# Kernel optimization log

Measured on AMD Instinct MI355X. Metric: run time of the kernel, lower is better.

## Reference

```python
import jax, jax.numpy as jnp
import numpy as np


def _segment_sum(x):
    # x: (..., T). Returns (..., T, T) with [i, j] = sum_{j < k <= i} x[k] for i >= j, else -inf.
    T = x.shape[-1]
    lower = jnp.tril(jnp.ones((T, T), dtype=bool), -1)
    xx = jnp.where(lower, x[..., :, None], 0.0)  # [..., i, j] = x[..., i] for i > j
    seg = jnp.cumsum(xx, axis=-2)
    keep = jnp.tril(jnp.ones((T, T), dtype=bool), 0)
    return jnp.where(keep, seg, -jnp.inf)


def _ssd(x, dt, A, B, C, chunk_len, D):
    # x: (b,s,H,dh)  dt: (b,s,H)  A: (H,)  B,C: (b,s,H,N)
    b, s, H, dh = x.shape
    N = B.shape[-1]
    c = s // chunk_len  # seq_len multiple of chunk_len -> pad_size == 0
    D_res = D[..., None] * x
    x = x * dt[..., None]
    Adt = A.astype(x.dtype) * dt  # (b,s,H)
    xc = x.reshape(b, c, chunk_len, H, dh)
    Ac = Adt.reshape(b, c, chunk_len, H).transpose(0, 3, 1, 2)  # (b,H,c,L)
    Bc = B.reshape(b, c, chunk_len, H, N)
    Cc = C.reshape(b, c, chunk_len, H, N)
    A_cumsum = jnp.cumsum(Ac, axis=-1)  # (b,H,c,L)
    Lmat = jnp.exp(_segment_sum(Ac))  # (b,H,c,L,L)
    # intra-chunk (diagonal) term
    Gm = jnp.einsum('bclhn,bcshn->bclsh', Cc, Bc)
    M = Gm * Lmat.transpose(0, 2, 3, 4, 1)  # (b,c,L,L,H)
    Y_diag = jnp.einsum('bclsh,bcshd->bclhd', M, xc)
    # chunk states
    decay_states = jnp.exp(A_cumsum[..., -1:] - A_cumsum)  # (b,H,c,L)
    B_decay = Bc * decay_states.transpose(0, 2, 3, 1)[..., None]
    states = jnp.einsum('bclhn,bclhd->bchdn', B_decay, xc)  # (b,c,H,dh,N)
    states = jnp.concatenate([jnp.zeros_like(states[:, :1]), states], axis=1)  # (b,c+1,H,dh,N)
    decay_chunk = jnp.exp(_segment_sum(jnp.pad(A_cumsum[..., -1], ((0, 0), (0, 0), (1, 0)))))  # (b,H,c+1,c+1)
    # Faithful to the source module: (decay[...,None,None] * states[:, :, None]).sum(dim=2)
    # sums over the z (row) axis -> equivalent to scaling states by the column sums of decay_chunk.
    col_sum = decay_chunk.sum(axis=2)  # (b,H,c+1)
    new_states = states * col_sum.transpose(0, 2, 1)[..., None, None]  # (b,c+1,H,dh,N)
    states = new_states[:, :-1]  # (b,c,H,dh,N)
    # inter-chunk (off-diagonal) term
    Y_off = jnp.einsum('bclhn,bchdn->bclhd', Cc, states) * jnp.exp(A_cumsum).transpose(0, 2, 3, 1)[..., None]
    return (Y_diag + Y_off).reshape(b, s, H, dh) + D_res


def setup_inputs() -> dict:
    key = jax.random.key(0)
    ks = jax.random.split(key, 6)
    b, s, dm, H, N, G = 2, 2048, 2048, 32, 128, 8
    sc = 0.02
    return {
        'hidden_states': jax.random.normal(ks[0], (b, s, dm), jnp.float32),
        'A_log': jnp.log(jnp.arange(1, H + 1, dtype=jnp.float32)),
        'D': jnp.ones((H,), jnp.float32),
        'W_B': jax.random.normal(ks[1], (dm, G * N), jnp.float32) * sc,
        'b_B': jnp.zeros((G * N,), jnp.float32),
        'W_C': jax.random.normal(ks[2], (dm, G * N), jnp.float32) * sc,
        'b_C': jnp.zeros((G * N,), jnp.float32),
        'W_x': jax.random.normal(ks[3], (dm, dm), jnp.float32) * sc,
        'b_x': jnp.zeros((dm,), jnp.float32),
        'W_dt': jax.random.normal(ks[4], (dm, H), jnp.float32) * sc,
        'b_dt': jnp.zeros((H,), jnp.float32),
        'W_out': jax.random.normal(ks[5], (dm, dm), jnp.float32) * sc,
        'b_out': jnp.zeros((dm,), jnp.float32),
        'chunk_len': 256,
        'd_state': 128,
    }


def reference(hidden_states, A_log, D, W_B, b_B, W_C, b_C, W_x, b_x, W_dt, b_dt, W_out, b_out, chunk_len, d_state):
    b, s, dm = hidden_states.shape
    H = A_log.shape[0]
    G = W_B.shape[1] // d_state
    A = -jnp.exp(A_log)
    Bm = (hidden_states @ W_B + b_B).reshape(b, s, G, d_state)
    Bm = jnp.tile(Bm, (1, 1, H // G, 1))  # torch .repeat tiles groups over heads
    Cm = (hidden_states @ W_C + b_C).reshape(b, s, G, d_state)
    Cm = jnp.tile(Cm, (1, 1, H // G, 1))
    dt = jax.nn.softplus(hidden_states @ W_dt + b_dt)  # (b,s,H)
    x = (hidden_states @ W_x + b_x).reshape(b, s, H, dm // H)
    y = _ssd(x, dt, A, Bm, Cm, chunk_len, D)
    return y.reshape(b, s, dm) @ W_out + b_out
```

## Files before the change

### kernel.cpp

```cpp
#include <hip/hip_runtime.h>

#define S_   2048
#define BB   2
#define MR   4096
#define DM   2048
#define HH   32
#define DH   64
#define GG   8
#define NST  128
#define NC   8
#define LCH  256
#define KD   2048

typedef __attribute__((ext_vector_type(4))) float f32x4;
typedef __attribute__((ext_vector_type(8))) short bf16x8;

typedef __attribute__((address_space(1))) const void gvoid;
typedef __attribute__((address_space(3))) void lvoid;

__device__ __forceinline__ short f2bf(float f) {
  unsigned u = __builtin_bit_cast(unsigned, f);
  u += 0x7FFFu + ((u >> 16) & 1u);
  return (short)(u >> 16);
}
__device__ __forceinline__ float bf2f(short s) {
  unsigned u = ((unsigned)(unsigned short)s) << 16;
  return __builtin_bit_cast(float, u);
}
__device__ __forceinline__ unsigned pack2(short lo, short hi) {
  return (unsigned)(unsigned short)lo | ((unsigned)(unsigned short)hi << 16);
}

__global__ void k_cast(const float* __restrict__ src, short* __restrict__ dst, int n8) {
  int i = blockIdx.x * 256 + threadIdx.x;
  if (i >= n8) return;
  const float4 a = *(const float4*)(src + (size_t)i * 8);
  const float4 b = *(const float4*)(src + (size_t)i * 8 + 4);
  uint4 o;
  o.x = pack2(f2bf(a.x), f2bf(a.y));
  o.y = pack2(f2bf(a.z), f2bf(a.w));
  o.z = pack2(f2bf(b.x), f2bf(b.y));
  o.w = pack2(f2bf(b.z), f2bf(b.w));
  *(uint4*)(dst + (size_t)i * 8) = o;
}

__global__ __launch_bounds__(256) void k_cast_T(const float* __restrict__ src,
                                                short* __restrict__ dst, int K, int N) {
  __shared__ short t[32][33];
  int bx = blockIdx.x * 32, by = blockIdx.y * 32;
  int tx = threadIdx.x & 31, ty = threadIdx.x >> 5;
  for (int r = ty; r < 32; r += 8)
    t[r][tx] = f2bf(src[(size_t)(by + r) * N + bx + tx]);
  __syncthreads();
  for (int r = ty; r < 32; r += 8)
    dst[(size_t)(bx + r) * K + by + tx] = t[tx][r];
}

template <int OUT_BF16>
__global__ __launch_bounds__(256) void k_gemm(const short* __restrict__ A,
                                              const short* __restrict__ Bt,
                                              const float* __restrict__ bias,
                                              void* __restrict__ out, int M, int N, int K) {
  __shared__ short As[64 * 40];
  __shared__ short Bs[64 * 40];
  const int tid = threadIdx.x;
  const int bm = blockIdx.y * 64, bn = blockIdx.x * 64;
  const int wid = tid >> 6, lane = tid & 63, lg = lane >> 4, lr = lane & 15;
  const int wr = wid >> 1, wc = wid & 1;
  const int arow = tid >> 2, aseg = (tid & 3) * 8;
  const bool bok = (bn + arow) < N;
  const short* Arow = A + (size_t)(bm + arow) * K + aseg;
  const short* Brow = Bt + (size_t)(bn + arow) * K + aseg;
  f32x4 acc[2][2] = {};
  for (int k0 = 0; k0 < K; k0 += 32) {
    uint4 av = *(const uint4*)(Arow + k0);
    uint4 bv;
    if (bok) bv = *(const uint4*)(Brow + k0);
    else     bv = make_uint4(0u, 0u, 0u, 0u);
    __syncthreads();
    *(uint4*)(As + arow * 40 + aseg) = av;
    *(uint4*)(Bs + arow * 40 + aseg) = bv;
    __syncthreads();
    bf16x8 af0 = *(const bf16x8*)(As + (wr * 32 + lr) * 40 + lg * 8);
    bf16x8 af1 = *(const bf16x8*)(As + (wr * 32 + 16 + lr) * 40 + lg * 8);
    bf16x8 bf0 = *(const bf16x8*)(Bs + (wc * 32 + lr) * 40 + lg * 8);
    bf16x8 bf1 = *(const bf16x8*)(Bs + (wc * 32 + 16 + lr) * 40 + lg * 8);
    acc[0][0] = __builtin_amdgcn_mfma_f32_16x16x32_bf16(af0, bf0, acc[0][0], 0, 0, 0);
    acc[0][1] = __builtin_amdgcn_mfma_f32_16x16x32_bf16(af0, bf1, acc[0][1], 0, 0, 0);
    acc[1][0] = __builtin_amdgcn_mfma_f32_16x16x32_bf16(af1, bf0, acc[1][0], 0, 0, 0);
    acc[1][1] = __builtin_amdgcn_mfma_f32_16x16x32_bf16(af1, bf1, acc[1][1], 0, 0, 0);
  }
  for (int mi = 0; mi < 2; ++mi)
    for (int ni = 0; ni < 2; ++ni) {
      int col = bn + wc * 32 + ni * 16 + lr;
      if (col >= N) continue;
      float bv = bias[col];
      int row0 = bm + wr * 32 + mi * 16 + lg * 4;
      for (int r = 0; r < 4; ++r) {
        float v = acc[mi][ni][r] + bv;
        if (OUT_BF16) ((short*)out)[(size_t)(row0 + r) * N + col] = f2bf(v);
        else          ((float*)out)[(size_t)(row0 + r) * N + col] = v;
      }
    }
}

template <int OUT_BF16>
__global__ __launch_bounds__(256) void k_gemm128(const short* __restrict__ A,
                                                 const short* __restrict__ Bt,
                                                 const float* __restrict__ bias,
                                                 void* __restrict__ out,
                                                 int M, int N, int K) {
  __shared__ short As[128 * 32];
  __shared__ short Bs[128 * 32];
  const int tid = threadIdx.x;
  const int bm = blockIdx.y * 128, bn = blockIdx.x * 128;
  const int wid = tid >> 6, lane = tid & 63, lg = lane >> 4, lr = lane & 15;
  const int wr = wid >> 1, wc = wid & 1;
  const int srow = tid >> 2, skseg = (tid & 3) * 8;
  const short* gA0 = A + (size_t)(bm + srow) * K + skseg;
  const short* gA1 = A + (size_t)(bm + 64 + srow) * K + skseg;
  const short* gB0 = Bt + (size_t)(bn + srow) * K + skseg;
  const short* gB1 = Bt + (size_t)(bn + 64 + srow) * K + skseg;
  char* lA = (char*)As + wid * 1024;
  char* lB = (char*)Bs + wid * 1024;
  f32x4 acc[4][4] = {};
  for (int k0 = 0; k0 < K; k0 += 32) {
    __syncthreads();
    __builtin_amdgcn_global_load_lds((gvoid*)(gA0 + k0), (lvoid*)lA, 16, 0, 0);
    __builtin_amdgcn_global_load_lds((gvoid*)(gA1 + k0), (lvoid*)(lA + 4096), 16, 0, 0);
    __builtin_amdgcn_global_load_lds((gvoid*)(gB0 + k0), (lvoid*)lB, 16, 0, 0);
    __builtin_amdgcn_global_load_lds((gvoid*)(gB1 + k0), (lvoid*)(lB + 4096), 16, 0, 0);
    __syncthreads();
    bf16x8 af[4], bfv[4];
    for (int mi = 0; mi < 4; ++mi)
      af[mi] = *(const bf16x8*)(As + (wr * 64 + mi * 16 + lr) * 32 + lg * 8);
    for (int ni = 0; ni < 4; ++ni)
      bfv[ni] = *(const bf16x8*)(Bs + (wc * 64 + ni * 16 + lr) * 32 + lg * 8);
    for (int mi = 0; mi < 4; ++mi)
      for (int ni = 0; ni < 4; ++ni)
        acc[mi][ni] = __builtin_amdgcn_mfma_f32_16x16x32_bf16(af[mi], bfv[ni], acc[mi][ni], 0, 0, 0);
  }
  for (int mi = 0; mi < 4; ++mi)
    for (int ni = 0; ni < 4; ++ni) {
      int col = bn + wc * 64 + ni * 16 + lr;
      float bv = bias[col];
      int row0 = bm + wr * 64 + mi * 16 + lg * 4;
      for (int r = 0; r < 4; ++r) {
        float v = acc[mi][ni][r] + bv;
        if (OUT_BF16) ((short*)out)[(size_t)(row0 + r) * N + col] = f2bf(v);
        else          ((float*)out)[(size_t)(row0 + r) * N + col] = v;
      }
    }
}

__global__ void k_dt(const float* __restrict__ dtraw, const float* __restrict__ A_log,
                     float* __restrict__ dtsp, float* __restrict__ adt, int n) {
  int i = blockIdx.x * 256 + threadIdx.x;
  if (i >= n) return;
  int h = i & (HH - 1);
  float z = dtraw[i];
  float sp = (z > 20.f) ? z : log1pf(expf(z));
  dtsp[i] = sp;
  adt[i] = -expf(A_log[h]) * sp;
}

__global__ void k_xdt(const float* __restrict__ xraw, const float* __restrict__ dtsp,
                      short* __restrict__ xbf, int n4) {
  int i = blockIdx.x * 256 + threadIdx.x;
  if (i >= n4) return;
  size_t e = (size_t)i * 4;
  int row = (int)(e >> 11);
  int col = (int)(e & (DM - 1));
  int h = col >> 6;
  float dt = dtsp[row * HH + h];
  float4 v = *(const float4*)(xraw + e);
  uint2 o;
  o.x = pack2(f2bf(v.x * dt), f2bf(v.y * dt));
  o.y = pack2(f2bf(v.z * dt), f2bf(v.w * dt));
  *(uint2*)(xbf + e) = o;
}

__global__ __launch_bounds__(256) void k_scan(const float* __restrict__ adt,
                                              float* __restrict__ acs,
                                              float* __restrict__ asum) {
  int blk = blockIdx.x;
  int h = blk & 31, ci = (blk >> 5) & 7, b = blk >> 8;
  int l = threadIdx.x;
  __shared__ float sc[256];
  sc[l] = adt[(size_t)(b * S_ + ci * LCH + l) * HH + h];
  __syncthreads();
  for (int o = 1; o < 256; o <<= 1) {
    float t = (l >= o) ? sc[l - o] : 0.f;
    float own = sc[l];
    __syncthreads();
    sc[l] = own + t;
    __syncthreads();
  }
  float r = sc[l];
  acs[((size_t)((b * HH + h) * NC + ci)) * LCH + l] = r;
  if (l == 255) asum[(b * HH + h) * NC + ci] = r;
}

__global__ void k_colsum(const float* __restrict__ asum, float* __restrict__ csum) {
  int t = threadIdx.x;
  if (t >= BB * HH) return;
  float av[NC];
  for (int k = 0; k < NC; ++k) av[k] = asum[t * NC + k];
  for (int z = 0; z < NC; ++z) {
    float run = 0.f, acc = 1.f;
    for (int j = z; j < NC; ++j) { run += av[j]; acc += __expf(run); }
    csum[t * NC + z] = acc;
  }
}

__global__ __launch_bounds__(256) void k_states(const short* __restrict__ Bbf,
                                                const short* __restrict__ xdt,
                                                const float* __restrict__ acs,
                                                const float* __restrict__ asum,
                                                short* __restrict__ state) {
  int blk = blockIdx.x;
  int h = blk & 31, ci = (blk >> 5) & 7, b = blk >> 8;
  int g = h & 7;
  int tid = threadIdx.x, wid = tid >> 6, lane = tid & 63, lg = lane >> 4, lr = lane & 15;
  __shared__ float dsh[256];
  __shared__ short Bt[128 * 40];
  __shared__ short Xt[64 * 40];
  const float* acs_p = acs + ((size_t)((b * HH + h) * NC + ci)) * LCH;
  float last = asum[(b * HH + h) * NC + ci];
  dsh[tid] = __expf(last - acs_p[tid]);
  const short* Bbase = Bbf + ((size_t)(b * S_ + ci * LCH) * GG + g) * NST;
  const short* Xbase = xdt + (size_t)(b * S_ + ci * LCH) * DM + h * DH;
  const int lrow = tid >> 3, nseg = (tid & 7) * 16, dseg = (tid & 7) * 8;
  f32x4 acc[2][4] = {};
  for (int l0 = 0; l0 < LCH; l0 += 32) {
    uint4 b0 = *(const uint4*)(Bbase + (size_t)(l0 + lrow) * (GG * NST) + nseg);
    uint4 b1 = *(const uint4*)(Bbase + (size_t)(l0 + lrow) * (GG * NST) + nseg + 8);
    uint4 xv = *(const uint4*)(Xbase + (size_t)(l0 + lrow) * DM + dseg);
    __syncthreads();
    float dly = dsh[l0 + lrow];
    const short* bp0 = (const short*)&b0;
    for (int e = 0; e < 8; ++e) Bt[(nseg + e) * 40 + lrow] = f2bf(bf2f(bp0[e]) * dly);
    const short* bp1 = (const short*)&b1;
    for (int e = 0; e < 8; ++e) Bt[(nseg + 8 + e) * 40 + lrow] = f2bf(bf2f(bp1[e]) * dly);
    const short* xp = (const short*)&xv;
    for (int e = 0; e < 8; ++e) Xt[(dseg + e) * 40 + lrow] = xp[e];
    __syncthreads();
    bf16x8 afr[2], bfr[4];
    for (int mi = 0; mi < 2; ++mi)
      afr[mi] = *(const bf16x8*)(Bt + (wid * 32 + mi * 16 + lr) * 40 + lg * 8);
    for (int ni = 0; ni < 4; ++ni)
      bfr[ni] = *(const bf16x8*)(Xt + (ni * 16 + lr) * 40 + lg * 8);
    for (int mi = 0; mi < 2; ++mi)
      for (int ni = 0; ni < 4; ++ni)
        acc[mi][ni] = __builtin_amdgcn_mfma_f32_16x16x32_bf16(afr[mi], bfr[ni], acc[mi][ni], 0, 0, 0);
  }
  short* sp = state + (size_t)blk * DH * NST;
  for (int mi = 0; mi < 2; ++mi)
    for (int ni = 0; ni < 4; ++ni)
      for (int r = 0; r < 4; ++r) {
        int n = wid * 32 + mi * 16 + lg * 4 + r;
        int d = ni * 16 + lr;
        sp[d * NST + n] = f2bf(acc[mi][ni][r]);
      }
}

__global__ __launch_bounds__(256) void k_y(const short* __restrict__ Cbf,
                                           const short* __restrict__ Bbf,
                                           const short* __restrict__ xdt,
                                           const float* __restrict__ xraw,
                                           const float* __restrict__ acs,
                                           const float* __restrict__ csum,
                                           const short* __restrict__ state,
                                           const float* __restrict__ Dv,
                                           short* __restrict__ Ybuf) {
  int blk = blockIdx.x;
  int h = blk & 31, ci = (blk >> 5) & 7, b = blk >> 8;
  int g = h & 7;
  int tid = threadIdx.x, wid = tid >> 6, lane = tid & 63, lg = lane >> 4, lr = lane & 15;
  __shared__ float ash[256];
  __shared__ short Xt[64 * 264];
  __shared__ short Mld[4][64 * 40];
  const float* acs_p = acs + ((size_t)((b * HH + h) * NC + ci)) * LCH;
  ash[tid] = acs_p[tid];
  float cs = csum[(b * HH + h) * NC + ci];
  const short* Xbase = xdt + (size_t)(b * S_ + ci * LCH) * DM + h * DH;
  {
    const short* xr = Xbase + (size_t)tid * DM;
    for (int d0 = 0; d0 < DH; d0 += 8) {
      uint4 v = *(const uint4*)(xr + d0);
      const short* vp = (const short*)&v;
      for (int e = 0; e < 8; ++e) Xt[(d0 + e) * 264 + tid] = vp[e];
    }
  }
  __syncthreads();
  f32x4 acc[4][4] = {};
  const short* Crow0 = Cbf + ((size_t)(b * S_ + ci * LCH) * GG + g) * NST;
  if (ci > 0) {
    const short* sp = state + (size_t)((b * NC + ci - 1) * HH + h) * DH * NST;
    for (int n0 = 0; n0 < NST; n0 += 32) {
      bf16x8 afr[4], bfr[4];
      for (int mi = 0; mi < 4; ++mi)
        afr[mi] = *(const bf16x8*)(Crow0 + (size_t)(wid * 64 + mi * 16 + lr) * (GG * NST) + n0 + lg * 8);
      for (int ni = 0; ni < 4; ++ni)
        bfr[ni] = *(const bf16x8*)(sp + (ni * 16 + lr) * NST + n0 + lg * 8);
      for (int mi = 0; mi < 4; ++mi)
        for (int ni = 0; ni < 4; ++ni)
          acc[mi][ni] = __builtin_amdgcn_mfma_f32_16x16x32_bf16(afr[mi], bfr[ni], acc[mi][ni], 0, 0, 0);
    }
    for (int mi = 0; mi < 4; ++mi)
      for (int r = 0; r < 4; ++r) {
        int i = wid * 64 + mi * 16 + lg * 4 + r;
        float f = __expf(ash[i]) * cs;
        for (int ni = 0; ni < 4; ++ni) acc[mi][ni][r] *= f;
      }
  }
  short* Ml = &Mld[wid][0];
  int jtmax = (wid * 64 + 63) >> 5;
  for (int jt = 0; jt <= jtmax; ++jt) {
    f32x4 gacc[4][2] = {};
    for (int n0 = 0; n0 < NST; n0 += 32) {
      bf16x8 afr[4], bfr[2];
      for (int mi = 0; mi < 4; ++mi)
        afr[mi] = *(const bf16x8*)(Crow0 + (size_t)(wid * 64 + mi * 16 + lr) * (GG * NST) + n0 + lg * 8);
      for (int nj = 0; nj < 2; ++nj) {
        int j = jt * 32 + nj * 16 + lr;
        bfr[nj] = *(const bf16x8*)(Bbf + ((size_t)(b * S_ + ci * LCH + j) * GG + g) * NST + n0 + lg * 8);
      }
      for (int mi = 0; mi < 4; ++mi)
        for (int nj = 0; nj < 2; ++nj)
          gacc[mi][nj] = __builtin_amdgcn_mfma_f32_16x16x32_bf16(afr[mi], bfr[nj], gacc[mi][nj], 0, 0, 0);
    }
    for (int mi = 0; mi < 4; ++mi)
      for (int nj = 0; nj < 2; ++nj)
        for (int r = 0; r < 4; ++r) {
          int i = wid * 64 + mi * 16 + lg * 4 + r;
          int jc = jt * 32 + nj * 16 + lr;
          float v = 0.f;
          if (jc <= i) v = gacc[mi][nj][r] * __expf(ash[i] - ash[jc]);
          Ml[(mi * 16 + lg * 4 + r) * 40 + nj * 16 + lr] = f2bf(v);
        }
    bf16x8 mfr[4], xfr[4];
    for (int mi = 0; mi < 4; ++mi) mfr[mi] = *(const bf16x8*)(Ml + (mi * 16 + lr) * 40 + lg * 8);
    for (int ni = 0; ni < 4; ++ni) xfr[ni] = *(const bf16x8*)(Xt + (ni * 16 + lr) * 264 + jt * 32 + lg * 8);
    for (int mi = 0; mi < 4; ++mi)
      for (int ni = 0; ni < 4; ++ni)
        acc[mi][ni] = __builtin_amdgcn_mfma_f32_16x16x32_bf16(mfr[mi], xfr[ni], acc[mi][ni], 0, 0, 0);
  }
  float Dh = Dv[h];
  const float* xr0 = xraw + (size_t)(b * S_ + ci * LCH) * DM + h * DH;
  short* yb = Ybuf + (size_t)(b * S_ + ci * LCH) * DM + h * DH;
  for (int mi = 0; mi < 4; ++mi)
    for (int r = 0; r < 4; ++r) {
      int i = wid * 64 + mi * 16 + lg * 4 + r;
      for (int ni = 0; ni < 4; ++ni) {
        int d = ni * 16 + lr;
        float v = acc[mi][ni][r] + Dh * xr0[(size_t)i * DM + d];
        yb[(size_t)i * DM + d] = f2bf(v);
      }
    }
}

extern "C" void kernel_launch(void* const* d_in, const int* in_sizes, int n_in,
                              void* d_out, int out_size, void* d_ws, size_t ws_size,
                              hipStream_t stream) {
  const float* hs    = (const float*)d_in[0];
  const float* A_log = (const float*)d_in[1];
  const float* Dv    = (const float*)d_in[2];
  const float* W_B   = (const float*)d_in[3];
  const float* b_B   = (const float*)d_in[4];
  const float* W_C   = (const float*)d_in[5];
  const float* b_C   = (const float*)d_in[6];
  const float* W_x   = (const float*)d_in[7];
  const float* b_x   = (const float*)d_in[8];
  const float* W_dt  = (const float*)d_in[9];
  const float* b_dt  = (const float*)d_in[10];
  const float* W_out = (const float*)d_in[11];
  const float* b_out = (const float*)d_in[12];

  char* w = (char*)d_ws;
  size_t off = 0;
  auto alloc = [&](size_t bytes) -> char* {
    char* p = w + off;
    off += (bytes + 255) & ~(size_t)255;
    return p;
  };
  short* hs_bf = (short*)alloc((size_t)MR * DM * 2);
  short* WxT   = (short*)alloc((size_t)DM * DM * 2);
  short* WBT   = (short*)alloc((size_t)1024 * DM * 2);
  short* WCT   = (short*)alloc((size_t)1024 * DM * 2);
  short* WdtT  = (short*)alloc((size_t)32 * DM * 2);
  short* WoutT = (short*)alloc((size_t)DM * DM * 2);
  float* xraw  = (float*)alloc((size_t)MR * DM * 4);
  short* Bbf   = (short*)alloc((size_t)MR * 1024 * 2);
  short* Cbf   = (short*)alloc((size_t)MR * 1024 * 2);
  float* dtraw = (float*)alloc((size_t)MR * HH * 4);
  float* dtsp  = (float*)alloc((size_t)MR * HH * 4);
  float* adt   = (float*)alloc((size_t)MR * HH * 4);
  float* acs   = (float*)alloc((size_t)BB * HH * NC * LCH * 4);
  float* asum  = (float*)alloc((size_t)BB * HH * NC * 4);
  float* csum  = (float*)alloc((size_t)BB * HH * NC * 4);
  short* state = (short*)alloc((size_t)BB * NC * HH * DH * NST * 2);
  short* xdtbf = (short*)alloc((size_t)MR * DM * 2);
  short* Ybuf  = (short*)alloc((size_t)MR * DM * 2);
  (void)ws_size; (void)in_sizes; (void)n_in; (void)out_size;

  k_cast<<<(MR * DM / 8 + 255) / 256, 256, 0, stream>>>(hs, hs_bf, MR * DM / 8);
  k_cast_T<<<dim3(DM / 32, DM / 32), 256, 0, stream>>>(W_x, WxT, DM, DM);
  k_cast_T<<<dim3(1024 / 32, DM / 32), 256, 0, stream>>>(W_B, WBT, DM, 1024);
  k_cast_T<<<dim3(1024 / 32, DM / 32), 256, 0, stream>>>(W_C, WCT, DM, 1024);
  k_cast_T<<<dim3(1, DM / 32), 256, 0, stream>>>(W_dt, WdtT, DM, 32);
  k_cast_T<<<dim3(DM / 32, DM / 32), 256, 0, stream>>>(W_out, WoutT, DM, DM);

  k_gemm<0><<<dim3(1, MR / 64), 256, 0, stream>>>(hs_bf, WdtT, b_dt, dtraw, MR, 32, KD);
  k_gemm128<0><<<dim3(DM / 128, MR / 128), 256, 0, stream>>>(hs_bf, WxT, b_x, xraw, MR, DM, KD);
  k_gemm128<1><<<dim3(1024 / 128, MR / 128), 256, 0, stream>>>(hs_bf, WBT, b_B, Bbf, MR, 1024, KD);
  k_gemm128<1><<<dim3(1024 / 128, MR / 128), 256, 0, stream>>>(hs_bf, WCT, b_C, Cbf, MR, 1024, KD);

  k_dt<<<(MR * HH + 255) / 256, 256, 0, stream>>>(dtraw, A_log, dtsp, adt, MR * HH);
  k_xdt<<<(MR * DM / 4 + 255) / 256, 256, 0, stream>>>(xraw, dtsp, xdtbf, MR * DM / 4);
  k_scan<<<BB * HH * NC, 256, 0, stream>>>(adt, acs, asum);
  k_colsum<<<1, 64, 0, stream>>>(asum, csum);

  k_states<<<BB * NC * HH, 256, 0, stream>>>(Bbf, xdtbf, acs, asum, state);
  k_y<<<BB * NC * HH, 256, 0, stream>>>(Cbf, Bbf, xdtbf, xraw, acs, csum, state, Dv, Ybuf);

  k_gemm128<0><<<dim3(DM / 128, MR / 128), 256, 0, stream>>>(Ybuf, WoutT, b_out, (float*)d_out, MR, DM, KD);
}
```

Baseline: 470.8 us.

## Fuse x/B/C projections into one concatenated GEMM with fused dt epilogue

```diff
diff --git a/kernel.cpp b/kernel.cpp
--- a/kernel.cpp
+++ b/kernel.cpp
@@ -11,6 +11,7 @@
 #define NC   8
 #define LCH  256
 #define KD   2048
+#define NCAT 4096
 
 typedef __attribute__((ext_vector_type(4))) float f32x4;
 typedef __attribute__((ext_vector_type(8))) short bf16x8;
@@ -29,6 +30,16 @@
 }
 __device__ __forceinline__ unsigned pack2(short lo, short hi) {
   return (unsigned)(unsigned short)lo | ((unsigned)(unsigned short)hi << 16);
+}
+
+__device__ __forceinline__ void xcd_swz(int& bx, int& by) {
+  int nx = gridDim.x;
+  int nwg = nx * gridDim.y;
+  int bid = by * nx + bx;
+  int q = nwg >> 3;
+  int wg = (bid & 7) * q + (bid >> 3);
+  bx = wg % nx;
+  by = wg / nx;
 }
 
 __global__ void k_cast(const float* __restrict__ src, short* __restrict__ dst, int n8) {
@@ -56,11 +67,21 @@
     dst[(size_t)(bx + r) * K + by + tx] = t[tx][r];
 }
 
-template <int OUT_BF16>
-__global__ __launch_bounds__(256) void k_gemm(const short* __restrict__ A,
-                                              const short* __restrict__ Bt,
-                                              const float* __restrict__ bias,
-                                              void* __restrict__ out, int M, int N, int K) {
+__global__ void k_biascat(const float* __restrict__ bx, const float* __restrict__ bb,
+                          const float* __restrict__ bc, float* __restrict__ out) {
+  int i = blockIdx.x * 256 + threadIdx.x;
+  if (i >= NCAT) return;
+  float v;
+  if (i < 2048) v = bx[i];
+  else if (i < 3072) v = bb[i - 2048];
+  else v = bc[i - 3072];
+  out[i] = v;
+}
+
+__global__ __launch_bounds__(256) void k_gemm64(const short* __restrict__ A,
+                                                const short* __restrict__ Bt,
+                                                const float* __restrict__ bias,
+                                                float* __restrict__ out, int M, int N, int K) {
   __shared__ short As[64 * 40];
   __shared__ short Bs[64 * 40];
   const int tid = threadIdx.x;
@@ -96,24 +117,87 @@
       if (col >= N) continue;
       float bv = bias[col];
       int row0 = bm + wr * 32 + mi * 16 + lg * 4;
-      for (int r = 0; r < 4; ++r) {
-        float v = acc[mi][ni][r] + bv;
-        if (OUT_BF16) ((short*)out)[(size_t)(row0 + r) * N + col] = f2bf(v);
-        else          ((float*)out)[(size_t)(row0 + r) * N + col] = v;
+      for (int r = 0; r < 4; ++r)
+        out[(size_t)(row0 + r) * N + col] = acc[mi][ni][r] + bv;
+    }
+}
+
+__global__ __launch_bounds__(256) void k_projcat(const short* __restrict__ A,
+                                                 const short* __restrict__ Bt,
+                                                 const float* __restrict__ bias,
+                                                 const float* __restrict__ dtsp,
+                                                 short* __restrict__ xbf,
+                                                 short* __restrict__ xdtbf,
+                                                 short* __restrict__ Bbf,
+                                                 short* __restrict__ Cbf) {
+  __shared__ short As[128 * 32];
+  __shared__ short Bs[128 * 32];
+  int bx = blockIdx.x, by = blockIdx.y;
+  xcd_swz(bx, by);
+  const int tid = threadIdx.x;
+  const int bm = by * 128, bn = bx * 128;
+  const int wid = tid >> 6, lane = tid & 63, lg = lane >> 4, lr = lane & 15;
+  const int wr = wid >> 1, wc = wid & 1;
+  const int srow = tid >> 2, skseg = (tid & 3) * 8;
+  const short* gA0 = A + (size_t)(bm + srow) * KD + skseg;
+  const short* gA1 = A + (size_t)(bm + 64 + srow) * KD + skseg;
+  const short* gB0 = Bt + (size_t)(bn + srow) * KD + skseg;
+  const short* gB1 = Bt + (size_t)(bn + 64 + srow) * KD + skseg;
+  char* lA = (char*)As + wid * 1024;
+  char* lB = (char*)Bs + wid * 1024;
+  f32x4 acc[4][4] = {};
+  for (int k0 = 0; k0 < KD; k0 += 32) {
+    __syncthreads();
+    __builtin_amdgcn_global_load_lds((gvoid*)(gA0 + k0), (lvoid*)lA, 16, 0, 0);
+    __builtin_amdgcn_global_load_lds((gvoid*)(gA1 + k0), (lvoid*)(lA + 4096), 16, 0, 0);
+    __builtin_amdgcn_global_load_lds((gvoid*)(gB0 + k0), (lvoid*)lB, 16, 0, 0);
+    __builtin_amdgcn_global_load_lds((gvoid*)(gB1 + k0), (lvoid*)(lB + 4096), 16, 0, 0);
+    __syncthreads();
+    bf16x8 af[4], bfv[4];
+    for (int mi = 0; mi < 4; ++mi)
+      af[mi] = *(const bf16x8*)(As + (wr * 64 + mi * 16 + lr) * 32 + lg * 8);
+    for (int ni = 0; ni < 4; ++ni)
+      bfv[ni] = *(const bf16x8*)(Bs + (wc * 64 + ni * 16 + lr) * 32 + lg * 8);
+    for (int mi = 0; mi < 4; ++mi)
+      for (int ni = 0; ni < 4; ++ni)
+        acc[mi][ni] = __builtin_amdgcn_mfma_f32_16x16x32_bf16(af[mi], bfv[ni], acc[mi][ni], 0, 0, 0);
+  }
+  for (int mi = 0; mi < 4; ++mi)
+    for (int ni = 0; ni < 4; ++ni) {
+      int colg = bn + wc * 64 + ni * 16 + lr;
+      float bv = bias[colg];
+      int row0 = bm + wr * 64 + mi * 16 + lg * 4;
+      if (bn < 2048) {
+        int h = colg >> 6;
+        for (int r = 0; r < 4; ++r) {
+          int row = row0 + r;
+          float v = acc[mi][ni][r] + bv;
+          xbf[(size_t)row * DM + colg] = f2bf(v);
+          xdtbf[(size_t)row * DM + colg] = f2bf(v * dtsp[row * HH + h]);
+        }
+      } else if (bn < 3072) {
+        int c2 = colg - 2048;
+        for (int r = 0; r < 4; ++r)
+          Bbf[(size_t)(row0 + r) * 1024 + c2] = f2bf(acc[mi][ni][r] + bv);
+      } else {
+        int c2 = colg - 3072;
+        for (int r = 0; r < 4; ++r)
+          Cbf[(size_t)(row0 + r) * 1024 + c2] = f2bf(acc[mi][ni][r] + bv);
       }
     }
 }
 
-template <int OUT_BF16>
 __global__ __launch_bounds__(256) void k_gemm128(const short* __restrict__ A,
                                                  const short* __restrict__ Bt,
                                                  const float* __restrict__ bias,
-                                                 void* __restrict__ out,
+                                                 float* __restrict__ out,
                                                  int M, int N, int K) {
   __shared__ short As[128 * 32];
   __shared__ short Bs[128 * 32];
+  int bx = blockIdx.x, by = blockIdx.y;
+  xcd_swz(bx, by);
   const int tid = threadIdx.x;
-  const int bm = blockIdx.y * 128, bn = blockIdx.x * 128;
+  const int bm = by * 128, bn = bx * 128;
   const int wid = tid >> 6, lane = tid & 63, lg = lane >> 4, lr = lane & 15;
   const int wr = wid >> 1, wc = wid & 1;
   const int srow = tid >> 2, skseg = (tid & 3) * 8;
@@ -145,11 +229,8 @@
       int col = bn + wc * 64 + ni * 16 + lr;
       float bv = bias[col];
       int row0 = bm + wr * 64 + mi * 16 + lg * 4;
-      for (int r = 0; r < 4; ++r) {
-        float v = acc[mi][ni][r] + bv;
-        if (OUT_BF16) ((short*)out)[(size_t)(row0 + r) * N + col] = f2bf(v);
-        else          ((float*)out)[(size_t)(row0 + r) * N + col] = v;
-      }
+      for (int r = 0; r < 4; ++r)
+        out[(size_t)(row0 + r) * N + col] = acc[mi][ni][r] + bv;
     }
 }
 
@@ -162,22 +243,6 @@
   float sp = (z > 20.f) ? z : log1pf(expf(z));
   dtsp[i] = sp;
   adt[i] = -expf(A_log[h]) * sp;
-}
-
-__global__ void k_xdt(const float* __restrict__ xraw, const float* __restrict__ dtsp,
-                      short* __restrict__ xbf, int n4) {
-  int i = blockIdx.x * 256 + threadIdx.x;
-  if (i >= n4) return;
-  size_t e = (size_t)i * 4;
-  int row = (int)(e >> 11);
-  int col = (int)(e & (DM - 1));
-  int h = col >> 6;
-  float dt = dtsp[row * HH + h];
-  float4 v = *(const float4*)(xraw + e);
-  uint2 o;
-  o.x = pack2(f2bf(v.x * dt), f2bf(v.y * dt));
-  o.y = pack2(f2bf(v.z * dt), f2bf(v.w * dt));
-  *(uint2*)(xbf + e) = o;
 }
 
 __global__ __launch_bounds__(256) void k_scan(const float* __restrict__ adt,
@@ -267,7 +332,7 @@
 __global__ __launch_bounds__(256) void k_y(const short* __restrict__ Cbf,
                                            const short* __restrict__ Bbf,
                                            const short* __restrict__ xdt,
-                                           const float* __restrict__ xraw,
+                                           const short* __restrict__ xbf,
                                            const float* __restrict__ acs,
                                            const float* __restrict__ csum,
                                            const short* __restrict__ state,
@@ -347,14 +412,14 @@
         acc[mi][ni] = __builtin_amdgcn_mfma_f32_16x16x32_bf16(mfr[mi], xfr[ni], acc[mi][ni], 0, 0, 0);
   }
   float Dh = Dv[h];
-  const float* xr0 = xraw + (size_t)(b * S_ + ci * LCH) * DM + h * DH;
+  const short* xr0 = xbf + (size_t)(b * S_ + ci * LCH) * DM + h * DH;
   short* yb = Ybuf + (size_t)(b * S_ + ci * LCH) * DM + h * DH;
   for (int mi = 0; mi < 4; ++mi)
     for (int r = 0; r < 4; ++r) {
       int i = wid * 64 + mi * 16 + lg * 4 + r;
       for (int ni = 0; ni < 4; ++ni) {
         int d = ni * 16 + lr;
-        float v = acc[mi][ni][r] + Dh * xr0[(size_t)i * DM + d];
+        float v = acc[mi][ni][r] + Dh * bf2f(xr0[(size_t)i * DM + d]);
         yb[(size_t)i * DM + d] = f2bf(v);
       }
     }
@@ -384,45 +449,44 @@
     off += (bytes + 255) & ~(size_t)255;
     return p;
   };
-  short* hs_bf = (short*)alloc((size_t)MR * DM * 2);
-  short* WxT   = (short*)alloc((size_t)DM * DM * 2);
-  short* WBT   = (short*)alloc((size_t)1024 * DM * 2);
-  short* WCT   = (short*)alloc((size_t)1024 * DM * 2);
-  short* WdtT  = (short*)alloc((size_t)32 * DM * 2);
-  short* WoutT = (short*)alloc((size_t)DM * DM * 2);
-  float* xraw  = (float*)alloc((size_t)MR * DM * 4);
-  short* Bbf   = (short*)alloc((size_t)MR * 1024 * 2);
-  short* Cbf   = (short*)alloc((size_t)MR * 1024 * 2);
-  float* dtraw = (float*)alloc((size_t)MR * HH * 4);
-  float* dtsp  = (float*)alloc((size_t)MR * HH * 4);
-  float* adt   = (float*)alloc((size_t)MR * HH * 4);
-  float* acs   = (float*)alloc((size_t)BB * HH * NC * LCH * 4);
-  float* asum  = (float*)alloc((size_t)BB * HH * NC * 4);
-  float* csum  = (float*)alloc((size_t)BB * HH * NC * 4);
-  short* state = (short*)alloc((size_t)BB * NC * HH * DH * NST * 2);
-  short* xdtbf = (short*)alloc((size_t)MR * DM * 2);
-  short* Ybuf  = (short*)alloc((size_t)MR * DM * 2);
+  short* hs_bf  = (short*)alloc((size_t)MR * DM * 2);
+  short* WcatT  = (short*)alloc((size_t)NCAT * KD * 2);
+  short* WdtT   = (short*)alloc((size_t)32 * KD * 2);
+  short* WoutT  = (short*)alloc((size_t)DM * KD * 2);
+  float* biascat= (float*)alloc((size_t)NCAT * 4);
+  short* xbf    = (short*)alloc((size_t)MR * DM * 2);
+  short* Bbf    = (short*)alloc((size_t)MR * 1024 * 2);
+  short* Cbf    = (short*)alloc((size_t)MR * 1024 * 2);
+  float* dtraw  = (float*)alloc((size_t)MR * HH * 4);
+  float* dtsp   = (float*)alloc((size_t)MR * HH * 4);
+  float* adt    = (float*)alloc((size_t)MR * HH * 4);
+  float* acs    = (float*)alloc((size_t)BB * HH * NC * LCH * 4);
+  float* asum   = (float*)alloc((size_t)BB * HH * NC * 4);
+  float* csum   = (float*)alloc((size_t)BB * HH * NC * 4);
+  short* state  = (short*)alloc((size_t)BB * NC * HH * DH * NST * 2);
+  short* xdtbf  = (short*)alloc((size_t)MR * DM * 2);
+  short* Ybuf   = (short*)alloc((size_t)MR * DM * 2);
   (void)ws_size; (void)in_sizes; (void)n_in; (void)out_size;
 
   k_cast<<<(MR * DM / 8 + 255) / 256, 256, 0, stream>>>(hs, hs_bf, MR * DM / 8);
-  k_cast_T<<<dim3(DM / 32, DM / 32), 256, 0, stream>>>(W_x, WxT, DM, DM);
-  k_cast_T<<<dim3(1024 / 32, DM / 32), 256, 0, stream>>>(W_B, WBT, DM, 1024);
-  k_cast_T<<<dim3(1024 / 32, DM / 32), 256, 0, stream>>>(W_C, WCT, DM, 1024);
-  k_cast_T<<<dim3(1, DM / 32), 256, 0, stream>>>(W_dt, WdtT, DM, 32);
-  k_cast_T<<<dim3(DM / 32, DM / 32), 256, 0, stream>>>(W_out, WoutT, DM, DM);
-
-  k_gemm<0><<<dim3(1, MR / 64), 256, 0, stream>>>(hs_bf, WdtT, b_dt, dtraw, MR, 32, KD);
-  k_gemm128<0><<<dim3(DM / 128, MR / 128), 256, 0, stream>>>(hs_bf, WxT, b_x, xraw, MR, DM, KD);
-  k_gemm128<1><<<dim3(1024 / 128, MR / 128), 256, 0, stream>>>(hs_bf, WBT, b_B, Bbf, MR, 1024, KD);
-  k_gemm128<1><<<dim3(1024 / 128, MR / 128), 256, 0, stream>>>(hs_bf, WCT, b_C, Cbf, MR, 1024, KD);
-
+  k_cast_T<<<dim3(DM / 32, KD / 32), 256, 0, stream>>>(W_x, WcatT, KD, DM);
+  k_cast_T<<<dim3(1024 / 32, KD / 32), 256, 0, stream>>>(W_B, WcatT + (size_t)2048 * KD, KD, 1024);
+  k_cast_T<<<dim3(1024 / 32, KD / 32), 256, 0, stream>>>(W_C, WcatT + (size_t)3072 * KD, KD, 1024);
+  k_cast_T<<<dim3(1, KD / 32), 256, 0, stream>>>(W_dt, WdtT, KD, 32);
+  k_cast_T<<<dim3(DM / 32, KD / 32), 256, 0, stream>>>(W_out, WoutT, KD, DM);
+  k_biascat<<<(NCAT + 255) / 256, 256, 0, stream>>>(b_x, b_B, b_C, biascat);
+
+  k_gemm64<<<dim3(1, MR / 64), 256, 0, stream>>>(hs_bf, WdtT, b_dt, dtraw, MR, 32, KD);
   k_dt<<<(MR * HH + 255) / 256, 256, 0, stream>>>(dtraw, A_log, dtsp, adt, MR * HH);
-  k_xdt<<<(MR * DM / 4 + 255) / 256, 256, 0, stream>>>(xraw, dtsp, xdtbf, MR * DM / 4);
+
+  k_projcat<<<dim3(NCAT / 128, MR / 128), 256, 0, stream>>>(hs_bf, WcatT, biascat, dtsp,
+                                                            xbf, xdtbf, Bbf, Cbf);
+
   k_scan<<<BB * HH * NC, 256, 0, stream>>>(adt, acs, asum);
   k_colsum<<<1, 64, 0, stream>>>(asum, csum);
 
   k_states<<<BB * NC * HH, 256, 0, stream>>>(Bbf, xdtbf, acs, asum, state);
-  k_y<<<BB * NC * HH, 256, 0, stream>>>(Cbf, Bbf, xdtbf, xraw, acs, csum, state, Dv, Ybuf);
-
-  k_gemm128<0><<<dim3(DM / 128, MR / 128), 256, 0, stream>>>(Ybuf, WoutT, b_out, (float*)d_out, MR, DM, KD);
-}
+  k_y<<<BB * NC * HH, 256, 0, stream>>>(Cbf, Bbf, xdtbf, xbf, acs, csum, state, Dv, Ybuf);
+
+  k_gemm128<<<dim3(DM / 128, MR / 128), 256, 0, stream>>>(Ybuf, WoutT, b_out, (float*)d_out, MR, DM, KD);
+}
```

Result: slower. 1.338 ms (+184.1%).
